# Kernel optimization log

Hardware: AMD Instinct MI355X
Metric: run time of the kernel (lower is better)

Reference implementation:

```python
import jax, jax.numpy as jnp
import numpy as np

N = 100000
E = 1600000
H = 128
M = 256
L = 6
G = 512          # number of graphs in the batch
A = 95           # num_atom_types
EXTRA = 3        # input_dim - 1
EPS = 1e-5


def swish(x):
    return x * jax.nn.sigmoid(x)


def setup_inputs() -> dict:
    key = jax.random.key(0)
    ks = jax.random.split(key, 16)
    z = jax.random.randint(ks[0], (N, 1), 0, A).astype(jnp.float32)
    extra = jax.random.normal(ks[1], (N, EXTRA), dtype=jnp.float32)
    x = jnp.concatenate([z, extra], axis=1)                     # [N, 4]
    edge_index = jax.random.randint(ks[2], (2, E), 0, N)        # [2, E]
    batch = jnp.sort(jax.random.randint(ks[3], (N,), 0, G))     # [N]
    s = 0.02
    z_embed = jax.random.normal(ks[4], (A, H), dtype=jnp.float32) * s
    extra_w = jax.random.normal(ks[5], (H, EXTRA), dtype=jnp.float32) * (1.0 / np.sqrt(EXTRA))
    extra_b = jnp.zeros((H,), jnp.float32)
    conv_w = jax.random.normal(ks[6], (L, H, H), dtype=jnp.float32) * (1.0 / np.sqrt(H))
    conv_b = jnp.zeros((L, H), jnp.float32)
    gamma = jnp.ones((L, H), jnp.float32)
    beta = jnp.zeros((L, H), jnp.float32)
    mean_scale = jnp.ones((L, H), jnp.float32)
    mlp_w1 = jax.random.normal(ks[7], (L, M, H), dtype=jnp.float32) * (1.0 / np.sqrt(H))
    mlp_b1 = jnp.zeros((L, M), jnp.float32)
    mlp_w2 = jax.random.normal(ks[8], (L, H, M), dtype=jnp.float32) * (1.0 / np.sqrt(M))
    mlp_b2 = jnp.zeros((L, H), jnp.float32)
    return dict(x=x, edge_index=edge_index, batch=batch, z_embed=z_embed,
                extra_w=extra_w, extra_b=extra_b, conv_w=conv_w, conv_b=conv_b,
                gamma=gamma, beta=beta, mean_scale=mean_scale,
                mlp_w1=mlp_w1, mlp_b1=mlp_b1, mlp_w2=mlp_w2, mlp_b2=mlp_b2)


def gnn_forward(x, edge_index, batch, z_embed, extra_w, extra_b, conv_w, conv_b,
                gamma, beta, mean_scale, mlp_w1, mlp_b1, mlp_w2, mlp_b2):
    z = x[:, 0].astype(jnp.int32)
    h = z_embed[z] + x[:, 1:] @ extra_w.T + extra_b                 # [N, H]

    # GCN: add self loops, symmetric normalization (computed once; graph is static)
    loop = jnp.arange(N)
    src = jnp.concatenate([edge_index[0], loop])
    dst = jnp.concatenate([edge_index[1], loop])
    deg = jax.ops.segment_sum(jnp.ones_like(dst, jnp.float32), dst, num_segments=N)
    dinv = jnp.where(deg > 0, jax.lax.rsqrt(jnp.maximum(deg, 1.0)), 0.0)
    norm = (dinv[src] * dinv[dst])[:, None]                         # [E+N, 1]

    cnt = jax.ops.segment_sum(jnp.ones((N,), jnp.float32), batch, num_segments=G)[:, None]
    cnt = jnp.maximum(cnt, 1.0)

    for i in range(L):
        h_res = h
        # GCNConv
        xw = h @ conv_w[i].T
        agg = jax.ops.segment_sum(xw[src] * norm, dst, num_segments=N) + conv_b[i]
        # GraphNorm: gamma * (x - alpha*mean) / sqrt(var + eps) + beta, per graph
        mean = jax.ops.segment_sum(agg, batch, num_segments=G) / cnt   # [G, H]
        sub = agg - mean_scale[i] * mean[batch]
        var = jax.ops.segment_sum(sub * sub, batch, num_segments=G) / cnt
        hn = gamma[i] * sub * jax.lax.rsqrt(var[batch] + EPS) + beta[i]
        ha = swish(hn)
        # residual MLP
        h = swish(swish(ha @ mlp_w1[i].T + mlp_b1[i]) @ mlp_w2[i].T + mlp_b2[i]) + h_res
    return h


def reference(x, edge_index, batch, z_embed, extra_w, extra_b, conv_w, conv_b,
              gamma, beta, mean_scale, mlp_w1, mlp_b1, mlp_w2, mlp_b2):
    return gnn_forward(x, edge_index, batch, z_embed, extra_w, extra_b, conv_w, conv_b,
                       gamma, beta, mean_scale, mlp_w1, mlp_b1, mlp_w2, mlp_b2)
```

## Files before the change

kernel.cpp:

```cpp
#include <hip/hip_runtime.h>

#define NN 100000
#define EE 1600000
#define HH 128
#define MM 256
#define LL 6
#define GG 512
#define SCAN_NB ((NN + 1023) / 1024)

typedef __attribute__((ext_vector_type(8))) short short8;
typedef __attribute__((ext_vector_type(4))) float floatx4;

__device__ __forceinline__ float swishf(float v) {
    return v / (1.0f + __expf(-v));
}

__device__ __forceinline__ unsigned short f2bf(float f) {
    unsigned u = __builtin_bit_cast(unsigned, f);
    unsigned r = u + 0x7FFFu + ((u >> 16) & 1u);
    return (unsigned short)(r >> 16);
}

__device__ __forceinline__ float2 bf2f2(unsigned u) {
    float2 r;
    r.x = __builtin_bit_cast(float, u << 16);
    r.y = __builtin_bit_cast(float, u & 0xFFFF0000u);
    return r;
}

__global__ void k_embed(const float* __restrict__ x, const float* __restrict__ z_embed,
                        const float* __restrict__ ew, const float* __restrict__ eb,
                        float* __restrict__ h, unsigned short* __restrict__ hb) {
    int idx = blockIdx.x * blockDim.x + threadIdx.x;
    if (idx >= NN * 32) return;
    int n = idx >> 5;
    int c0 = (idx & 31) << 2;
    const float* xr = x + (size_t)n * 4;
    int z = (int)xr[0];
    float x1 = xr[1], x2 = xr[2], x3 = xr[3];
    const float* ze = z_embed + (size_t)z * HH + c0;
    float o[4];
#pragma unroll
    for (int j = 0; j < 4; ++j) {
        int c = c0 + j;
        o[j] = ze[j] + x1 * ew[c * 3 + 0] + x2 * ew[c * 3 + 1] + x3 * ew[c * 3 + 2] + eb[c];
    }
    *(float4*)(h + (size_t)n * HH + c0) = make_float4(o[0], o[1], o[2], o[3]);
    uint2 p;
    p.x = (unsigned)f2bf(o[0]) | ((unsigned)f2bf(o[1]) << 16);
    p.y = (unsigned)f2bf(o[2]) | ((unsigned)f2bf(o[3]) << 16);
    *(uint2*)(hb + (size_t)n * HH + c0) = p;
}

__global__ void k_f2bf(const float* __restrict__ src, unsigned short* __restrict__ dst, int n) {
    int i = blockIdx.x * blockDim.x + threadIdx.x;
    if (i < n) dst[i] = f2bf(src[i]);
}

__global__ void k_degree(const int* __restrict__ dst, int* __restrict__ deg) {
    int e = blockIdx.x * blockDim.x + threadIdx.x;
    if (e < EE) atomicAdd(&deg[dst[e]], 1);
}

__global__ void k_dinv(const int* __restrict__ deg, float* __restrict__ dinv) {
    int n = blockIdx.x * blockDim.x + threadIdx.x;
    if (n < NN) dinv[n] = rsqrtf((float)(deg[n] + 1));
}

__global__ void k_scan1(const int* __restrict__ deg, int* __restrict__ bsum) {
    __shared__ int sd[256];
    int t = threadIdx.x;
    int base = blockIdx.x * 1024 + t * 4;
    int s = 0;
#pragma unroll
    for (int j = 0; j < 4; ++j) {
        int i = base + j;
        if (i < NN) s += deg[i];
    }
    sd[t] = s;
    __syncthreads();
    for (int off = 128; off > 0; off >>= 1) {
        if (t < off) sd[t] += sd[t + off];
        __syncthreads();
    }
    if (t == 0) bsum[blockIdx.x] = sd[0];
}

__global__ void k_scan2(const int* __restrict__ bsum, int* __restrict__ boff) {
    __shared__ int sd[128];
    int t = threadIdx.x;
    int v = (t < SCAN_NB) ? bsum[t] : 0;
    sd[t] = v;
    __syncthreads();
    for (int off = 1; off < 128; off <<= 1) {
        int u = (t >= off) ? sd[t - off] : 0;
        __syncthreads();
        sd[t] += u;
        __syncthreads();
    }
    boff[t] = sd[t] - v;
}

__global__ void k_scan3(const int* __restrict__ deg, const int* __restrict__ boff,
                        int* __restrict__ rowptr) {
    __shared__ int sd[256];
    int t = threadIdx.x;
    int base = blockIdx.x * 1024 + t * 4;
    int v[4];
    int s = 0;
#pragma unroll
    for (int j = 0; j < 4; ++j) {
        int i = base + j;
        v[j] = (i < NN) ? deg[i] : 0;
        s += v[j];
    }
    sd[t] = s;
    __syncthreads();
    for (int off = 1; off < 256; off <<= 1) {
        int u = (t >= off) ? sd[t - off] : 0;
        __syncthreads();
        sd[t] += u;
        __syncthreads();
    }
    int run = boff[blockIdx.x] + sd[t] - s;
#pragma unroll
    for (int j = 0; j < 4; ++j) {
        int i = base + j;
        if (i < NN) rowptr[i] = run;
        if (i == NN - 1) rowptr[NN] = run + v[j];
        run += v[j];
    }
}

__global__ void k_fill(const int* __restrict__ ei, const int* __restrict__ rowptr,
                       int* __restrict__ cursor, int* __restrict__ col) {
    int e = blockIdx.x * blockDim.x + threadIdx.x;
    if (e >= EE) return;
    int s = ei[e];
    int d = ei[EE + e];
    int p = atomicAdd(&cursor[d], 1);
    col[rowptr[d] + p] = s;
}

__global__ void k_gptr(const int* __restrict__ batch, int* __restrict__ gptr) {
    int n = blockIdx.x * blockDim.x + threadIdx.x;
    if (n >= NN) return;
    int b = batch[n];
    int pb = (n == 0) ? -1 : batch[n - 1];
    for (int g = pb + 1; g <= b; ++g) gptr[g] = n;
    if (n == NN - 1) {
        for (int g = b + 1; g <= GG; ++g) gptr[g] = NN;
    }
}

template <int EPI>
__global__ __launch_bounds__(256) void k_gemm_mfma(const unsigned short* __restrict__ A,
                                                   const unsigned short* __restrict__ B,
                                                   const float* __restrict__ bias,
                                                   const float* aux, float* Cf,
                                                   unsigned short* __restrict__ Cb, int K,
                                                   int Cout) {
    __shared__ unsigned short As[128][72];
    __shared__ unsigned short Bs[128][72];
    const int tid = threadIdx.x;
    const int wave = tid >> 6;
    const int lane = tid & 63;
    const int quad = lane >> 4;
    const int l16 = lane & 15;
    const int wr = (wave & 1) << 6;
    const int wc = (wave >> 1) << 6;
    const int rowBase = blockIdx.x * 128;
    const int colBase = blockIdx.y * 128;

    floatx4 acc[4][4];
    const floatx4 zed = {0.f, 0.f, 0.f, 0.f};
#pragma unroll
    for (int i = 0; i < 4; ++i)
#pragma unroll
        for (int j = 0; j < 4; ++j) acc[i][j] = zed;

    const int srow = tid >> 3;
    const int skk = (tid & 7) << 3;

    for (int k0 = 0; k0 < K; k0 += 64) {
        __syncthreads();
#pragma unroll
        for (int p = 0; p < 4; ++p) {
            int rl = srow + (p << 5);
            int r = rowBase + rl;
            if (r >= NN) r = NN - 1;
            uint4 va = *(const uint4*)(A + (size_t)r * K + k0 + skk);
            *(uint4*)(&As[rl][skk]) = va;
            uint4 vb = *(const uint4*)(B + (size_t)(colBase + rl) * K + k0 + skk);
            *(uint4*)(&Bs[rl][skk]) = vb;
        }
        __syncthreads();
#pragma unroll
        for (int ks = 0; ks < 2; ++ks) {
            int koff = (ks << 5) + (quad << 3);
            short8 a[4], b[4];
#pragma unroll
            for (int i = 0; i < 4; ++i) a[i] = *(const short8*)(&As[wr + (i << 4) + l16][koff]);
#pragma unroll
            for (int j = 0; j < 4; ++j) b[j] = *(const short8*)(&Bs[wc + (j << 4) + l16][koff]);
#pragma unroll
            for (int i = 0; i < 4; ++i)
#pragma unroll
                for (int j = 0; j < 4; ++j)
                    acc[i][j] =
                        __builtin_amdgcn_mfma_f32_16x16x32_bf16(a[i], b[j], acc[i][j], 0, 0, 0);
        }
    }

    float bv[4];
    if (EPI >= 1) {
#pragma unroll
        for (int j = 0; j < 4; ++j) bv[j] = bias[colBase + wc + (j << 4) + l16];
    }
#pragma unroll
    for (int i = 0; i < 4; ++i) {
#pragma unroll
        for (int reg = 0; reg < 4; ++reg) {
            int r = rowBase + wr + (i << 4) + (quad << 2) + reg;
            if (r < NN) {
                if (EPI == 0) {
                    float dv = aux[r];
#pragma unroll
                    for (int j = 0; j < 4; ++j) {
                        int c = colBase + wc + (j << 4) + l16;
                        Cb[(size_t)r * Cout + c] = f2bf(acc[i][j][reg] * dv);
                    }
                } else if (EPI == 1) {
#pragma unroll
                    for (int j = 0; j < 4; ++j) {
                        int c = colBase + wc + (j << 4) + l16;
                        Cb[(size_t)r * Cout + c] = f2bf(swishf(acc[i][j][reg] + bv[j]));
                    }
                } else {
#pragma unroll
                    for (int j = 0; j < 4; ++j) {
                        int c = colBase + wc + (j << 4) + l16;
                        float o = swishf(acc[i][j][reg] + bv[j]) + aux[(size_t)r * HH + c];
                        Cf[(size_t)r * HH + c] = o;
                        Cb[(size_t)r * HH + c] = f2bf(o);
                    }
                }
            }
        }
    }
}

__global__ __launch_bounds__(256) void k_agg(const unsigned short* __restrict__ y,
                                             const int* __restrict__ rowptr,
                                             const int* __restrict__ col,
                                             const float* __restrict__ dinv,
                                             const float* __restrict__ cb,
                                             float* __restrict__ agg) {
    int w = threadIdx.x >> 6;
    int lane = threadIdx.x & 63;
    int d = blockIdx.x * 4 + w;
    if (d >= NN) return;
    int c = lane << 1;
    const unsigned* yv = (const unsigned*)y;
    float2 acc = bf2f2(yv[(size_t)d * 64 + lane]);
    int beg = rowptr[d];
    int end = rowptr[d + 1];
    int e = beg;
    for (; e + 3 < end; e += 4) {
        int s0 = col[e], s1 = col[e + 1], s2 = col[e + 2], s3 = col[e + 3];
        float2 v0 = bf2f2(yv[(size_t)s0 * 64 + lane]);
        float2 v1 = bf2f2(yv[(size_t)s1 * 64 + lane]);
        float2 v2 = bf2f2(yv[(size_t)s2 * 64 + lane]);
        float2 v3 = bf2f2(yv[(size_t)s3 * 64 + lane]);
        acc.x += (v0.x + v1.x) + (v2.x + v3.x);
        acc.y += (v0.y + v1.y) + (v2.y + v3.y);
    }
    for (; e < end; ++e) {
        float2 v0 = bf2f2(yv[(size_t)col[e] * 64 + lane]);
        acc.x += v0.x;
        acc.y += v0.y;
    }
    float dv = dinv[d];
    float2 outv;
    outv.x = acc.x * dv + cb[c];
    outv.y = acc.y * dv + cb[c + 1];
    *(float2*)(agg + (size_t)d * HH + c) = outv;
}

__global__ __launch_bounds__(512) void k_stats(const float* __restrict__ agg,
                                               const int* __restrict__ gptr,
                                               const float* __restrict__ ms,
                                               float* __restrict__ gmean,
                                               float* __restrict__ grstd) {
    __shared__ float s1[512];
    __shared__ float s2[512];
    int g = blockIdx.x;
    int t = threadIdx.x;
    int c = t & 127;
    int part = t >> 7;
    int beg = gptr[g];
    int end = gptr[g + 1];
    float S1 = 0.f, S2 = 0.f;
    for (int n = beg + part; n < end; n += 4) {
        float v = agg[(size_t)n * HH + c];
        S1 += v;
        S2 += v * v;
    }
    s1[t] = S1;
    s2[t] = S2;
    __syncthreads();
    if (part == 0) {
        S1 = (s1[c] + s1[c + 128]) + (s1[c + 256] + s1[c + 384]);
        S2 = (s2[c] + s2[c + 128]) + (s2[c + 256] + s2[c + 384]);
        int cnt = end - beg;
        float inv = 1.0f / (float)(cnt > 0 ? cnt : 1);
        float m = S1 * inv;
        float msc = ms[c];
        float var = S2 * inv - msc * (2.0f - msc) * m * m;
        gmean[g * HH + c] = m;
        grstd[g * HH + c] = rsqrtf(var + 1e-5f);
    }
}

__global__ void k_normswish(const float* __restrict__ agg, const int* __restrict__ batch,
                            const float* __restrict__ gamma, const float* __restrict__ beta,
                            const float* __restrict__ ms, const float* __restrict__ gmean,
                            const float* __restrict__ grstd, unsigned short* __restrict__ ha) {
    int idx = blockIdx.x * blockDim.x + threadIdx.x;
    if (idx >= NN * 32) return;
    int n = idx >> 5;
    int c0 = (idx & 31) << 2;
    int g = batch[n];
    float4 a = *(const float4*)(agg + (size_t)n * HH + c0);
    float av[4] = {a.x, a.y, a.z, a.w};
    unsigned short o[4];
#pragma unroll
    for (int j = 0; j < 4; ++j) {
        int c = c0 + j;
        float sub = av[j] - ms[c] * gmean[g * HH + c];
        float hn = gamma[c] * sub * grstd[g * HH + c] + beta[c];
        o[j] = f2bf(swishf(hn));
    }
    uint2 p;
    p.x = (unsigned)o[0] | ((unsigned)o[1] << 16);
    p.y = (unsigned)o[2] | ((unsigned)o[3] << 16);
    *(uint2*)(ha + (size_t)n * HH + c0) = p;
}

extern "C" void kernel_launch(void* const* d_in, const int* in_sizes, int n_in,
                              void* d_out, int out_size, void* d_ws, size_t ws_size,
                              hipStream_t stream) {
    const float* x = (const float*)d_in[0];
    const int* ei = (const int*)d_in[1];
    const int* batch = (const int*)d_in[2];
    const float* z_embed = (const float*)d_in[3];
    const float* extra_w = (const float*)d_in[4];
    const float* extra_b = (const float*)d_in[5];
    const float* conv_w = (const float*)d_in[6];
    const float* conv_b = (const float*)d_in[7];
    const float* gamma = (const float*)d_in[8];
    const float* beta = (const float*)d_in[9];
    const float* mean_scale = (const float*)d_in[10];
    const float* mlp_w1 = (const float*)d_in[11];
    const float* mlp_b1 = (const float*)d_in[12];
    const float* mlp_w2 = (const float*)d_in[13];
    const float* mlp_b2 = (const float*)d_in[14];
    float* h = (float*)d_out;

    char* wsB = (char*)d_ws;
    size_t off = 0;
    auto alloc = [&](size_t bytes) -> void* {
        void* p = (void*)(wsB + off);
        off = (off + bytes + 255) & ~(size_t)255;
        return p;
    };
    float* dinv = (float*)alloc((size_t)NN * 4);
    int* deg = (int*)alloc((size_t)NN * 4);
    int* cursor = (int*)alloc((size_t)NN * 4);
    int* rowptr = (int*)alloc((size_t)(NN + 1) * 4);
    int* bsum = (int*)alloc(128 * 4);
    int* boff = (int*)alloc(128 * 4);
    int* col = (int*)alloc((size_t)EE * 4);
    int* gptr = (int*)alloc((size_t)(GG + 1) * 4);
    float* gmean = (float*)alloc((size_t)GG * HH * 4);
    float* grstd = (float*)alloc((size_t)GG * HH * 4);
    unsigned short* wb = (unsigned short*)alloc((size_t)(LL * (HH * HH + MM * HH + HH * MM)) * 2);
    unsigned short* cwb = wb;
    unsigned short* w1b = wb + (size_t)LL * HH * HH;
    unsigned short* w2b = w1b + (size_t)LL * MM * HH;
    unsigned short* hb = (unsigned short*)alloc((size_t)NN * HH * 2);
    unsigned short* ybuf = (unsigned short*)alloc((size_t)NN * HH * 2);
    float* agg = (float*)alloc((size_t)NN * HH * 4);
    unsigned short* tb = (unsigned short*)agg;

    hipMemsetAsync(deg, 0, (size_t)NN * 4, stream);
    hipMemsetAsync(cursor, 0, (size_t)NN * 4, stream);

    k_embed<<<(NN * 32 + 255) / 256, 256, 0, stream>>>(x, z_embed, extra_w, extra_b, h, hb);
    {
        int n1 = LL * HH * HH, n2 = LL * MM * HH, n3 = LL * HH * MM;
        k_f2bf<<<(n1 + 255) / 256, 256, 0, stream>>>(conv_w, cwb, n1);
        k_f2bf<<<(n2 + 255) / 256, 256, 0, stream>>>(mlp_w1, w1b, n2);
        k_f2bf<<<(n3 + 255) / 256, 256, 0, stream>>>(mlp_w2, w2b, n3);
    }
    k_degree<<<(EE + 255) / 256, 256, 0, stream>>>(ei + EE, deg);
    k_dinv<<<(NN + 255) / 256, 256, 0, stream>>>(deg, dinv);
    k_scan1<<<SCAN_NB, 256, 0, stream>>>(deg, bsum);
    k_scan2<<<1, 128, 0, stream>>>(bsum, boff);
    k_scan3<<<SCAN_NB, 256, 0, stream>>>(deg, boff, rowptr);
    k_fill<<<(EE + 255) / 256, 256, 0, stream>>>(ei, rowptr, cursor, col);
    k_gptr<<<(NN + 255) / 256, 256, 0, stream>>>(batch, gptr);

    dim3 g1((NN + 127) / 128, 1);
    dim3 g2((NN + 127) / 128, 2);
    for (int i = 0; i < LL; ++i) {
        k_gemm_mfma<0><<<g1, 256, 0, stream>>>(hb, cwb + (size_t)i * HH * HH, nullptr, dinv,
                                               nullptr, ybuf, HH, HH);
        k_agg<<<(NN + 3) / 4, 256, 0, stream>>>(ybuf, rowptr, col, dinv,
                                                conv_b + (size_t)i * HH, agg);
        k_stats<<<GG, 512, 0, stream>>>(agg, gptr, mean_scale + (size_t)i * HH, gmean, grstd);
        k_normswish<<<(NN * 32 + 255) / 256, 256, 0, stream>>>(
            agg, batch, gamma + (size_t)i * HH, beta + (size_t)i * HH,
            mean_scale + (size_t)i * HH, gmean, grstd, ybuf);
        k_gemm_mfma<1><<<g2, 256, 0, stream>>>(ybuf, w1b + (size_t)i * MM * HH,
                                               mlp_b1 + (size_t)i * MM, nullptr, nullptr, tb,
                                               HH, MM);
        k_gemm_mfma<2><<<g1, 256, 0, stream>>>(tb, w2b + (size_t)i * HH * MM,
                                               mlp_b2 + (size_t)i * HH, h, h, hb, MM, HH);
    }
}
```

Measured before the change: 1.512 ms.

## Store aggregation and residual in bf16, partition CSR atomics, merge weight casts

Keeps the residual stream only as bf16 instead of also maintaining an fp32 copy, and writes the fp32 output only in the final layer. The aggregation buffer becomes bf16, which halves traffic in the agg, stats and normswish kernels, and the agg gather loop is unrolled to 8 edges. Degree counting and CSR fill now use grid-stride kernels that split destinations into 8 ranges for better atomic locality, and the three weight casts are merged into one launch. The residual accumulates bf16 rounding error across layers, which risks reduced accuracy.

```diff
diff --git a/kernel.cpp b/kernel.cpp
--- a/kernel.cpp
+++ b/kernel.cpp
@@ -21,6 +21,10 @@
     return (unsigned short)(r >> 16);
 }
 
+__device__ __forceinline__ float bf2f(unsigned short u) {
+    return __builtin_bit_cast(float, (unsigned)u << 16);
+}
+
 __device__ __forceinline__ float2 bf2f2(unsigned u) {
     float2 r;
     r.x = __builtin_bit_cast(float, u << 16);
@@ -30,7 +34,7 @@
 
 __global__ void k_embed(const float* __restrict__ x, const float* __restrict__ z_embed,
                         const float* __restrict__ ew, const float* __restrict__ eb,
-                        float* __restrict__ h, unsigned short* __restrict__ hb) {
+                        unsigned short* __restrict__ hb) {
     int idx = blockIdx.x * blockDim.x + threadIdx.x;
     if (idx >= NN * 32) return;
     int n = idx >> 5;
@@ -45,21 +49,36 @@
         int c = c0 + j;
         o[j] = ze[j] + x1 * ew[c * 3 + 0] + x2 * ew[c * 3 + 1] + x3 * ew[c * 3 + 2] + eb[c];
     }
-    *(float4*)(h + (size_t)n * HH + c0) = make_float4(o[0], o[1], o[2], o[3]);
     uint2 p;
     p.x = (unsigned)f2bf(o[0]) | ((unsigned)f2bf(o[1]) << 16);
     p.y = (unsigned)f2bf(o[2]) | ((unsigned)f2bf(o[3]) << 16);
     *(uint2*)(hb + (size_t)n * HH + c0) = p;
 }
 
-__global__ void k_f2bf(const float* __restrict__ src, unsigned short* __restrict__ dst, int n) {
+__global__ void k_f2bf3(const float* __restrict__ s1, unsigned short* __restrict__ d1, int n1,
+                        const float* __restrict__ s2, unsigned short* __restrict__ d2, int n2,
+                        const float* __restrict__ s3, unsigned short* __restrict__ d3, int n3) {
     int i = blockIdx.x * blockDim.x + threadIdx.x;
-    if (i < n) dst[i] = f2bf(src[i]);
-}
-
-__global__ void k_degree(const int* __restrict__ dst, int* __restrict__ deg) {
-    int e = blockIdx.x * blockDim.x + threadIdx.x;
-    if (e < EE) atomicAdd(&deg[dst[e]], 1);
+    if (i < n1) {
+        d1[i] = f2bf(s1[i]);
+    } else if (i < n1 + n2) {
+        d2[i - n1] = f2bf(s2[i - n1]);
+    } else if (i < n1 + n2 + n3) {
+        d3[i - n1 - n2] = f2bf(s3[i - n1 - n2]);
+    }
+}
+
+__global__ __launch_bounds__(256) void k_degree_p(const int* __restrict__ dst,
+                                                  int* __restrict__ deg) {
+    int part = blockIdx.x & 7;
+    int blk = blockIdx.x >> 3;
+    int nb = gridDim.x >> 3;
+    int lo = (int)((long long)part * NN / 8);
+    int hi = (int)((long long)(part + 1) * NN / 8);
+    for (int e = blk * 256 + threadIdx.x; e < EE; e += nb * 256) {
+        int d = dst[e];
+        if (d >= lo && d < hi) atomicAdd(&deg[d], 1);
+    }
 }
 
 __global__ void k_dinv(const int* __restrict__ deg, float* __restrict__ dinv) {
@@ -132,14 +151,22 @@
     }
 }
 
-__global__ void k_fill(const int* __restrict__ ei, const int* __restrict__ rowptr,
-                       int* __restrict__ cursor, int* __restrict__ col) {
-    int e = blockIdx.x * blockDim.x + threadIdx.x;
-    if (e >= EE) return;
-    int s = ei[e];
-    int d = ei[EE + e];
-    int p = atomicAdd(&cursor[d], 1);
-    col[rowptr[d] + p] = s;
+__global__ __launch_bounds__(256) void k_fill_p(const int* __restrict__ ei,
+                                                const int* __restrict__ rowptr,
+                                                int* __restrict__ cursor,
+                                                int* __restrict__ col) {
+    int part = blockIdx.x & 7;
+    int blk = blockIdx.x >> 3;
+    int nb = gridDim.x >> 3;
+    int lo = (int)((long long)part * NN / 8);
+    int hi = (int)((long long)(part + 1) * NN / 8);
+    for (int e = blk * 256 + threadIdx.x; e < EE; e += nb * 256) {
+        int d = ei[EE + e];
+        if (d >= lo && d < hi) {
+            int p = atomicAdd(&cursor[d], 1);
+            col[rowptr[d] + p] = ei[e];
+        }
+    }
 }
 
 __global__ void k_gptr(const int* __restrict__ batch, int* __restrict__ gptr) {
@@ -157,9 +184,9 @@
 __global__ __launch_bounds__(256) void k_gemm_mfma(const unsigned short* __restrict__ A,
                                                    const unsigned short* __restrict__ B,
                                                    const float* __restrict__ bias,
-                                                   const float* aux, float* Cf,
+                                                   const void* aux, float* Cf,
                                                    unsigned short* __restrict__ Cb, int K,
-                                                   int Cout) {
+                                                   int Cout, int writeF) {
     __shared__ unsigned short As[128][72];
     __shared__ unsigned short Bs[128][72];
     const int tid = threadIdx.x;
@@ -224,7 +251,7 @@
             int r = rowBase + wr + (i << 4) + (quad << 2) + reg;
             if (r < NN) {
                 if (EPI == 0) {
-                    float dv = aux[r];
+                    float dv = ((const float*)aux)[r];
 #pragma unroll
                     for (int j = 0; j < 4; ++j) {
                         int c = colBase + wc + (j << 4) + l16;
@@ -237,12 +264,13 @@
                         Cb[(size_t)r * Cout + c] = f2bf(swishf(acc[i][j][reg] + bv[j]));
                     }
                 } else {
+                    const unsigned short* res = (const unsigned short*)aux;
 #pragma unroll
                     for (int j = 0; j < 4; ++j) {
                         int c = colBase + wc + (j << 4) + l16;
-                        float o = swishf(acc[i][j][reg] + bv[j]) + aux[(size_t)r * HH + c];
-                        Cf[(size_t)r * HH + c] = o;
+                        float o = swishf(acc[i][j][reg] + bv[j]) + bf2f(res[(size_t)r * HH + c]);
                         Cb[(size_t)r * HH + c] = f2bf(o);
+                        if (writeF) Cf[(size_t)r * HH + c] = o;
                     }
                 }
             }
@@ -255,7 +283,7 @@
                                              const int* __restrict__ col,
                                              const float* __restrict__ dinv,
                                              const float* __restrict__ cb,
-                                             float* __restrict__ agg) {
+                                             unsigned short* __restrict__ agg) {
     int w = threadIdx.x >> 6;
     int lane = threadIdx.x & 63;
     int d = blockIdx.x * 4 + w;
@@ -266,14 +294,18 @@
     int beg = rowptr[d];
     int end = rowptr[d + 1];
     int e = beg;
-    for (; e + 3 < end; e += 4) {
-        int s0 = col[e], s1 = col[e + 1], s2 = col[e + 2], s3 = col[e + 3];
-        float2 v0 = bf2f2(yv[(size_t)s0 * 64 + lane]);
-        float2 v1 = bf2f2(yv[(size_t)s1 * 64 + lane]);
-        float2 v2 = bf2f2(yv[(size_t)s2 * 64 + lane]);
-        float2 v3 = bf2f2(yv[(size_t)s3 * 64 + lane]);
-        acc.x += (v0.x + v1.x) + (v2.x + v3.x);
-        acc.y += (v0.y + v1.y) + (v2.y + v3.y);
+    for (; e + 7 < end; e += 8) {
+        int s[8];
+#pragma unroll
+        for (int q = 0; q < 8; ++q) s[q] = col[e + q];
+        float2 v[8];
+#pragma unroll
+        for (int q = 0; q < 8; ++q) v[q] = bf2f2(yv[(size_t)s[q] * 64 + lane]);
+#pragma unroll
+        for (int q = 0; q < 8; ++q) {
+            acc.x += v[q].x;
+            acc.y += v[q].y;
+        }
     }
     for (; e < end; ++e) {
         float2 v0 = bf2f2(yv[(size_t)col[e] * 64 + lane]);
@@ -281,13 +313,13 @@
         acc.y += v0.y;
     }
     float dv = dinv[d];
-    float2 outv;
-    outv.x = acc.x * dv + cb[c];
-    outv.y = acc.y * dv + cb[c + 1];
-    *(float2*)(agg + (size_t)d * HH + c) = outv;
-}
-
-__global__ __launch_bounds__(512) void k_stats(const float* __restrict__ agg,
+    float ox = acc.x * dv + cb[c];
+    float oy = acc.y * dv + cb[c + 1];
+    unsigned pk = (unsigned)f2bf(ox) | ((unsigned)f2bf(oy) << 16);
+    ((unsigned*)agg)[(size_t)d * 64 + lane] = pk;
+}
+
+__global__ __launch_bounds__(512) void k_stats(const unsigned short* __restrict__ agg,
                                                const int* __restrict__ gptr,
                                                const float* __restrict__ ms,
                                                float* __restrict__ gmean,
@@ -302,7 +334,7 @@
     int end = gptr[g + 1];
     float S1 = 0.f, S2 = 0.f;
     for (int n = beg + part; n < end; n += 4) {
-        float v = agg[(size_t)n * HH + c];
+        float v = bf2f(agg[(size_t)n * HH + c]);
         S1 += v;
         S2 += v * v;
     }
@@ -322,17 +354,20 @@
     }
 }
 
-__global__ void k_normswish(const float* __restrict__ agg, const int* __restrict__ batch,
-                            const float* __restrict__ gamma, const float* __restrict__ beta,
-                            const float* __restrict__ ms, const float* __restrict__ gmean,
-                            const float* __restrict__ grstd, unsigned short* __restrict__ ha) {
+__global__ void k_normswish(const unsigned short* __restrict__ agg,
+                            const int* __restrict__ batch, const float* __restrict__ gamma,
+                            const float* __restrict__ beta, const float* __restrict__ ms,
+                            const float* __restrict__ gmean, const float* __restrict__ grstd,
+                            unsigned short* __restrict__ ha) {
     int idx = blockIdx.x * blockDim.x + threadIdx.x;
     if (idx >= NN * 32) return;
     int n = idx >> 5;
     int c0 = (idx & 31) << 2;
     int g = batch[n];
-    float4 a = *(const float4*)(agg + (size_t)n * HH + c0);
-    float av[4] = {a.x, a.y, a.z, a.w};
+    uint2 ain = *(const uint2*)(agg + (size_t)n * HH + c0);
+    float2 a01 = bf2f2(ain.x);
+    float2 a23 = bf2f2(ain.y);
+    float av[4] = {a01.x, a01.y, a23.x, a23.y};
     unsigned short o[4];
 #pragma unroll
     for (int j = 0; j < 4; ++j) {
@@ -365,7 +400,7 @@
     const float* mlp_b1 = (const float*)d_in[12];
     const float* mlp_w2 = (const float*)d_in[13];
     const float* mlp_b2 = (const float*)d_in[14];
-    float* h = (float*)d_out;
+    float* h_out = (float*)d_out;
 
     char* wsB = (char*)d_ws;
     size_t off = 0;
@@ -384,48 +419,50 @@
     int* gptr = (int*)alloc((size_t)(GG + 1) * 4);
     float* gmean = (float*)alloc((size_t)GG * HH * 4);
     float* grstd = (float*)alloc((size_t)GG * HH * 4);
-    unsigned short* wb = (unsigned short*)alloc((size_t)(LL * (HH * HH + MM * HH + HH * MM)) * 2);
+    unsigned short* wb =
+        (unsigned short*)alloc((size_t)(LL * (HH * HH + MM * HH + HH * MM)) * 2);
     unsigned short* cwb = wb;
     unsigned short* w1b = wb + (size_t)LL * HH * HH;
     unsigned short* w2b = w1b + (size_t)LL * MM * HH;
     unsigned short* hb = (unsigned short*)alloc((size_t)NN * HH * 2);
     unsigned short* ybuf = (unsigned short*)alloc((size_t)NN * HH * 2);
-    float* agg = (float*)alloc((size_t)NN * HH * 4);
-    unsigned short* tb = (unsigned short*)agg;
+    unsigned short* tb = (unsigned short*)alloc((size_t)NN * MM * 2);
+    unsigned short* aggb = tb;
 
     hipMemsetAsync(deg, 0, (size_t)NN * 4, stream);
     hipMemsetAsync(cursor, 0, (size_t)NN * 4, stream);
 
-    k_embed<<<(NN * 32 + 255) / 256, 256, 0, stream>>>(x, z_embed, extra_w, extra_b, h, hb);
+    k_embed<<<(NN * 32 + 255) / 256, 256, 0, stream>>>(x, z_embed, extra_w, extra_b, hb);
     {
         int n1 = LL * HH * HH, n2 = LL * MM * HH, n3 = LL * HH * MM;
-        k_f2bf<<<(n1 + 255) / 256, 256, 0, stream>>>(conv_w, cwb, n1);
-        k_f2bf<<<(n2 + 255) / 256, 256, 0, stream>>>(mlp_w1, w1b, n2);
-        k_f2bf<<<(n3 + 255) / 256, 256, 0, stream>>>(mlp_w2, w2b, n3);
-    }
-    k_degree<<<(EE + 255) / 256, 256, 0, stream>>>(ei + EE, deg);
+        int nt = n1 + n2 + n3;
+        k_f2bf3<<<(nt + 255) / 256, 256, 0, stream>>>(conv_w, cwb, n1, mlp_w1, w1b, n2,
+                                                      mlp_w2, w2b, n3);
+    }
+    k_degree_p<<<1024, 256, 0, stream>>>(ei + EE, deg);
     k_dinv<<<(NN + 255) / 256, 256, 0, stream>>>(deg, dinv);
     k_scan1<<<SCAN_NB, 256, 0, stream>>>(deg, bsum);
     k_scan2<<<1, 128, 0, stream>>>(bsum, boff);
     k_scan3<<<SCAN_NB, 256, 0, stream>>>(deg, boff, rowptr);
-    k_fill<<<(EE + 255) / 256, 256, 0, stream>>>(ei, rowptr, cursor, col);
+    k_fill_p<<<1024, 256, 0, stream>>>(ei, rowptr, cursor, col);
     k_gptr<<<(NN + 255) / 256, 256, 0, stream>>>(batch, gptr);
 
     dim3 g1((NN + 127) / 128, 1);
     dim3 g2((NN + 127) / 128, 2);
     for (int i = 0; i < LL; ++i) {
         k_gemm_mfma<0><<<g1, 256, 0, stream>>>(hb, cwb + (size_t)i * HH * HH, nullptr, dinv,
-                                               nullptr, ybuf, HH, HH);
+                                               nullptr, ybuf, HH, HH, 0);
         k_agg<<<(NN + 3) / 4, 256, 0, stream>>>(ybuf, rowptr, col, dinv,
-                                                conv_b + (size_t)i * HH, agg);
-        k_stats<<<GG, 512, 0, stream>>>(agg, gptr, mean_scale + (size_t)i * HH, gmean, grstd);
+                                                conv_b + (size_t)i * HH, aggb);
+        k_stats<<<GG, 512, 0, stream>>>(aggb, gptr, mean_scale + (size_t)i * HH, gmean, grstd);
         k_normswish<<<(NN * 32 + 255) / 256, 256, 0, stream>>>(
-            agg, batch, gamma + (size_t)i * HH, beta + (size_t)i * HH,
+            aggb, batch, gamma + (size_t)i * HH, beta + (size_t)i * HH,
             mean_scale + (size_t)i * HH, gmean, grstd, ybuf);
         k_gemm_mfma<1><<<g2, 256, 0, stream>>>(ybuf, w1b + (size_t)i * MM * HH,
                                                mlp_b1 + (size_t)i * MM, nullptr, nullptr, tb,
-                                               HH, MM);
+                                               HH, MM, 0);
         k_gemm_mfma<2><<<g1, 256, 0, stream>>>(tb, w2b + (size_t)i * HH * MM,
-                                               mlp_b2 + (size_t)i * HH, h, h, hb, MM, HH);
-    }
-}
+                                               mlp_b2 + (size_t)i * HH, hb, h_out, hb, MM, HH,
+                                               i == LL - 1 ? 1 : 0);
+    }
+}
```

After: 1.429 ms. 1.06x faster.
